# Kernel tuning notes

Measured on AMD Instinct MI355X. Metric: run time of the kernel, lower is better.

The kernel has to match this reference:

```python
import jax, jax.numpy as jnp
import numpy as np

# ---- static config ----
B, H, W, C = 32, 64, 64, 256
WS, SHIFT, NH = 8, 4, 8
HD = C // NH
N = WS * WS  # tokens per window
NW = (H // WS) * (W // WS)
EPS = 1e-5


def _relative_position_index(ws):
    ch, cw = np.meshgrid(np.arange(ws), np.arange(ws), indexing='ij')
    coords = np.stack([ch, cw]).reshape(2, -1)          # (2, N)
    rel = coords[:, :, None] - coords[:, None, :]        # (2, N, N)
    rel = rel.transpose(1, 2, 0)
    rel[:, :, 0] += ws - 1
    rel[:, :, 1] += ws - 1
    rel[:, :, 0] *= 2 * ws - 1
    return jnp.asarray(rel.sum(-1))                      # (N, N) int


def _shifted_window_mask(h, w, ws, shift):
    img = np.zeros((h, w))
    slices = (slice(0, -ws), slice(-ws, -shift), slice(-shift, None))
    cnt = 0
    for hs in slices:
        for wsl in slices:
            img[hs, wsl] = cnt
            cnt += 1
    mw = img.reshape(h // ws, ws, w // ws, ws).transpose(0, 2, 1, 3).reshape(-1, ws * ws)
    diff = mw[:, None, :] - mw[:, :, None]
    return jnp.asarray(np.where(diff != 0, -100.0, 0.0).astype(np.float32))  # (nW, N, N)


REL_IDX = _relative_position_index(WS)
ATTN_MASK = _shifted_window_mask(H, W, WS, SHIFT)


def _layernorm(x, g, b):
    mu = jnp.mean(x, axis=-1, keepdims=True)
    var = jnp.mean(jnp.square(x - mu), axis=-1, keepdims=True)
    return (x - mu) * jax.lax.rsqrt(var + EPS) * g + b


def _window_partition(x):  # (B,H,W,C) -> (B*nW, N, C)
    x = x.reshape(B, H // WS, WS, W // WS, WS, C)
    return x.transpose(0, 1, 3, 2, 4, 5).reshape(-1, N, C)


def _window_reverse(win):  # (B*nW, N, C) -> (B,H,W,C)
    x = win.reshape(B, H // WS, W // WS, WS, WS, C)
    return x.transpose(0, 1, 3, 2, 4, 5).reshape(B, H, W, C)


def setup_inputs() -> dict:
    key = jax.random.key(0)
    ks = jax.random.split(key, 6)
    s = lambda fan_in: 1.0 / np.sqrt(fan_in)
    return {
        'x': jax.random.normal(ks[0], (B, H * W, C), jnp.float32),
        'norm1_g': jnp.ones((C,), jnp.float32),
        'norm1_b': jnp.zeros((C,), jnp.float32),
        'qkv_w': jax.random.normal(ks[1], (C, 3 * C), jnp.float32) * s(C),
        'qkv_b': jnp.zeros((3 * C,), jnp.float32),
        'proj_w': jax.random.normal(ks[2], (C, C), jnp.float32) * s(C),
        'proj_b': jnp.zeros((C,), jnp.float32),
        'bias_table': jax.random.normal(ks[3], ((2 * WS - 1) ** 2, NH), jnp.float32) * 0.02,
        'norm2_g': jnp.ones((C,), jnp.float32),
        'norm2_b': jnp.zeros((C,), jnp.float32),
        'fc1_w': jax.random.normal(ks[4], (C, 4 * C), jnp.float32) * s(C),
        'fc1_b': jnp.zeros((4 * C,), jnp.float32),
        'fc2_w': jax.random.normal(ks[5], (4 * C, C), jnp.float32) * s(4 * C),
        'fc2_b': jnp.zeros((C,), jnp.float32),
    }


def reference(x, norm1_g, norm1_b, qkv_w, qkv_b, proj_w, proj_b, bias_table,
              norm2_g, norm2_b, fc1_w, fc1_b, fc2_w, fc2_b):
    shortcut = x
    h = _layernorm(x, norm1_g, norm1_b).reshape(B, H, W, C)
    # cyclic shift
    h = jnp.roll(h, shift=(-SHIFT, -SHIFT), axis=(1, 2))
    xw = _window_partition(h)                               # (Bw, N, C), Bw = B*nW
    # window attention
    qkv = xw @ qkv_w + qkv_b                                 # (Bw, N, 3C)
    qkv = qkv.reshape(-1, N, 3, NH, HD).transpose(2, 0, 3, 1, 4)
    q, k, v = qkv[0], qkv[1], qkv[2]                         # (Bw, NH, N, HD)
    attn = jnp.einsum('whnd,whmd->whnm', q * (HD ** -0.5), k)
    rpb = bias_table[REL_IDX.reshape(-1)].reshape(N, N, NH).transpose(2, 0, 1)
    attn = attn + rpb[None]
    attn = attn.reshape(B, NW, NH, N, N) + ATTN_MASK[None, :, None]
    attn = jax.nn.softmax(attn.reshape(-1, NH, N, N), axis=-1)
    out = jnp.einsum('whnm,whmd->whnd', attn, v)
    out = out.transpose(0, 2, 1, 3).reshape(-1, N, C)
    out = out @ proj_w + proj_b
    # reverse windows + shift back
    h = _window_reverse(out)
    h = jnp.roll(h, shift=(SHIFT, SHIFT), axis=(1, 2)).reshape(B, H * W, C)
    x = shortcut + h
    # MLP with pre-norm residual
    m = _layernorm(x, norm2_g, norm2_b)
    m = jax.nn.gelu(m @ fc1_w + fc1_b, approximate=False) @ fc2_w + fc2_b
    return x + m
```

## Files before the change

### kernel.cpp

```cpp
#include <hip/hip_runtime.h>
#include <hip/hip_bf16.h>


typedef __bf16 bf16;
typedef __bf16 bf16x8 __attribute__((ext_vector_type(8)));
typedef __bf16 bf16x4 __attribute__((ext_vector_type(4)));
typedef float  f32x4  __attribute__((ext_vector_type(4)));

#define M_TOK 131072

#define GLDS(gp, lp)                                                                   \
    __builtin_amdgcn_global_load_lds(                                                  \
        (const __attribute__((address_space(1))) unsigned int*)(gp),                   \
        (__attribute__((address_space(3))) unsigned int*)(lp), 16, 0, 0)

__global__ __launch_bounds__(256) void transpose_w(const float* __restrict__ src,
                                                   bf16* __restrict__ dst,
                                                   int K, int N) {
    int idx = blockIdx.x * 256 + threadIdx.x;
    int k = idx / N, n = idx - k * N;
    dst[(size_t)n * K + k] = (bf16)src[idx];
}

__global__ __launch_bounds__(256) void build_rpb(const float* __restrict__ bt,
                                                 float* __restrict__ rpb) {
    int idx = blockIdx.x * 256 + threadIdx.x;
    int h = idx >> 12, n = (idx >> 6) & 63, m = idx & 63;
    int ridx = ((n >> 3) - (m >> 3) + 7) * 15 + ((n & 7) - (m & 7) + 7);
    rpb[idx] = bt[ridx * 8 + h];
}

template <int PERM>
__global__ __launch_bounds__(256) void ln_k(const float* __restrict__ x,
                                            const float* __restrict__ g,
                                            const float* __restrict__ bb,
                                            bf16* __restrict__ dst) {
    int t = blockIdx.x * 4 + (threadIdx.x >> 6);
    int lane = threadIdx.x & 63;
    size_t src;
    if (PERM) {
        int w = t >> 6, n = t & 63;
        int b = w >> 6, nw = w & 63;
        int r = ((nw >> 3) * 8 + (n >> 3) + 4) & 63;
        int c = ((nw & 7) * 8 + (n & 7) + 4) & 63;
        src = ((size_t)b * 4096 + r * 64 + c) * 256;
    } else {
        src = (size_t)t * 256;
    }
    float4 v = *(const float4*)&x[src + lane * 4];
    float s = v.x + v.y + v.z + v.w;
    float sq = v.x * v.x + v.y * v.y + v.z * v.z + v.w * v.w;
#pragma unroll
    for (int off = 1; off < 64; off <<= 1) {
        s += __shfl_xor(s, off);
        sq += __shfl_xor(sq, off);
    }
    float mean = s * (1.0f / 256.0f);
    float var = sq * (1.0f / 256.0f) - mean * mean;
    float rstd = rsqrtf(var + 1e-5f);
    float4 gg = *(const float4*)&g[lane * 4];
    float4 bv = *(const float4*)&bb[lane * 4];
    bf16x4 o;
    o[0] = (bf16)((v.x - mean) * rstd * gg.x + bv.x);
    o[1] = (bf16)((v.y - mean) * rstd * gg.y + bv.y);
    o[2] = (bf16)((v.z - mean) * rstd * gg.z + bv.z);
    o[3] = (bf16)((v.w - mean) * rstd * gg.w + bv.w);
    *(bf16x4*)&dst[(size_t)t * 256 + lane * 4] = o;
}

__device__ __forceinline__ float fast_gelu(float v) {
    float t = v * v;
    float w = __builtin_fmaf(0.044715f * t, v, v);
    float e = __expf(-1.5957691216057308f * w);
    return v * __builtin_amdgcn_rcpf(1.0f + e);
}

template <int NDIM, int KDIM, int EPI>
__global__ __launch_bounds__(256) void gemm_k(const bf16* __restrict__ A,
                                              const bf16* __restrict__ Bt,
                                              const float* __restrict__ bias,
                                              bf16* __restrict__ outb,
                                              float* __restrict__ outf,
                                              const float* __restrict__ resid) {
    __shared__ __align__(16) bf16 SH[24576];
    constexpr int NBN = NDIM / 128;
    constexpr int NK = KDIM / 32;
    static_assert(NK >= 3, "pipeline needs >=3 K-steps");
    const int tid = threadIdx.x;
    const int nwg = gridDim.x;
    const int flat = blockIdx.x;
    const int cpx = nwg >> 3;
    const int orig = (flat & 7) * cpx + (flat >> 3);
    const int bm = orig / NBN, bn = orig % NBN;

    const int lane = tid & 63, wid = tid >> 6;
    const int wr = wid >> 1, wc = wid & 1;
    const int lhi = lane >> 4, llo = lane & 15;

    f32x4 acc[4][4];
#pragma unroll
    for (int i = 0; i < 4; i++)
#pragma unroll
        for (int j = 0; j < 4; j++) acc[i][j] = f32x4{0.f, 0.f, 0.f, 0.f};

    const int srow = wid * 32 + (lane >> 2);
    const int scol = (((lane & 3) - ((lane >> 3) & 3)) & 3) * 8;
    const bf16* Ap = A + (size_t)(bm * 128 + srow) * KDIM + scol;
    const bf16* Bp = Bt + (size_t)(bn * 128 + srow) * KDIM + scol;
    const int gsw = ((lhi + (llo >> 1)) & 3) * 8;

#define STAGE(bufidx)                                                                  \
    do {                                                                               \
        bf16* Al = SH + (bufidx)*4096 + wid * 1024;                                    \
        bf16* Bl = SH + 12288 + (bufidx)*4096 + wid * 1024;                            \
        GLDS(Ap, Al);                                                                  \
        GLDS(Ap + 16 * KDIM, Al + 16 * 32);                                            \
        GLDS(Bp, Bl);                                                                  \
        GLDS(Bp + 16 * KDIM, Bl + 16 * 32);                                            \
        Ap += 32;                                                                      \
        Bp += 32;                                                                      \
    } while (0)

#define COMPUTE(bufidx)                                                                \
    do {                                                                               \
        const int ab = (bufidx)*4096;                                                  \
        bf16x8 af[4], bfr[4];                                                          \
        _Pragma("unroll") for (int mi = 0; mi < 4; mi++) af[mi] =                      \
            *(const bf16x8*)&SH[ab + (wr * 64 + mi * 16 + llo) * 32 + gsw];            \
        _Pragma("unroll") for (int ni = 0; ni < 4; ni++) bfr[ni] =                     \
            *(const bf16x8*)&SH[12288 + ab + (wc * 64 + ni * 16 + llo) * 32 + gsw];    \
        _Pragma("unroll") for (int mi = 0; mi < 4; mi++)                               \
            _Pragma("unroll") for (int ni = 0; ni < 4; ni++) acc[mi][ni] =             \
                __builtin_amdgcn_mfma_f32_16x16x32_bf16(bfr[ni], af[mi],               \
                                                        acc[mi][ni], 0, 0, 0);         \
    } while (0)

#define WAITBAR(N)                                                                     \
    asm volatile("s_waitcnt vmcnt(" #N ")" ::: "memory");                              \
    __builtin_amdgcn_s_barrier();                                                      \
    __builtin_amdgcn_sched_barrier(0)

#define END_PHASE                                                                      \
    asm volatile("s_waitcnt lgkmcnt(0)" ::: "memory");                                 \
    __builtin_amdgcn_s_barrier();                                                      \
    __builtin_amdgcn_sched_barrier(0)

    STAGE(0);
    STAGE(1);
    STAGE(2);
    int buf = 0;
    for (int i = 0; i + 3 < NK; ++i) {
        WAITBAR(8);
        COMPUTE(buf);
        END_PHASE;
        STAGE(buf);
        buf = (buf == 2) ? 0 : buf + 1;
    }
    WAITBAR(8);
    COMPUTE(buf);
    buf = (buf == 2) ? 0 : buf + 1;
    WAITBAR(4);
    COMPUTE(buf);
    buf = (buf == 2) ? 0 : buf + 1;
    WAITBAR(0);
    COMPUTE(buf);

#undef STAGE
#undef COMPUTE
#undef WAITBAR
#undef END_PHASE

    __syncthreads();

    char* shb = (char*)SH;
    if constexpr (EPI == 0 || EPI == 2) {
#pragma unroll
        for (int ni = 0; ni < 4; ni++) {
            const int lcol = wc * 64 + ni * 16 + lhi * 4;
            const float4 b4 = *(const float4*)&bias[bn * 128 + lcol];
#pragma unroll
            for (int mi = 0; mi < 4; mi++) {
                const int ltok = wr * 64 + mi * 16 + llo;
                float v0 = acc[mi][ni][0] + b4.x;
                float v1 = acc[mi][ni][1] + b4.y;
                float v2 = acc[mi][ni][2] + b4.z;
                float v3 = acc[mi][ni][3] + b4.w;
                bf16x4 o;
                if constexpr (EPI == 2) {
                    o[0] = (bf16)fast_gelu(v0); o[1] = (bf16)fast_gelu(v1);
                    o[2] = (bf16)fast_gelu(v2); o[3] = (bf16)fast_gelu(v3);
                } else {
                    o[0] = (bf16)v0; o[1] = (bf16)v1; o[2] = (bf16)v2; o[3] = (bf16)v3;
                }
                const int u2 = (lcol >> 3) ^ (ltok & 15);
                *(bf16x4*)(shb + ltok * 256 + u2 * 16 + (lcol & 7) * 2) = o;
            }
        }
        __syncthreads();
        const int j = lane & 15;
#pragma unroll
        for (int rnd = 0; rnd < 8; rnd++) {
            const int ltok = wid * 32 + rnd * 4 + (lane >> 4);
            const int u2 = j ^ (ltok & 15);
            bf16x8 v = *(const bf16x8*)(shb + ltok * 256 + u2 * 16);
            *(bf16x8*)&outb[(size_t)(bm * 128 + ltok) * NDIM + bn * 128 + j * 8] = v;
        }
    } else {
#pragma unroll
        for (int p = 0; p < 2; p++) {
            if (wc == p) {
#pragma unroll
                for (int ni = 0; ni < 4; ni++) {
                    const int lcolh = ni * 16 + lhi * 4;
                    const float4 b4 = *(const float4*)&bias[bn * 128 + p * 64 + lcolh];
#pragma unroll
                    for (int mi = 0; mi < 4; mi++) {
                        const int ltok = wr * 64 + mi * 16 + llo;
                        float4 o = {acc[mi][ni][0] + b4.x, acc[mi][ni][1] + b4.y,
                                    acc[mi][ni][2] + b4.z, acc[mi][ni][3] + b4.w};
                        const int u2 = (lcolh >> 2) ^ (ltok & 15);
                        *(float4*)(shb + ltok * 256 + u2 * 16) = o;
                    }
                }
            }
            __syncthreads();
            const int j = lane & 15;
#pragma unroll
            for (int rnd = 0; rnd < 8; rnd++) {
                const int ltok = wid * 32 + rnd * 4 + (lane >> 4);
                const int u2 = j ^ (ltok & 15);
                float4 v = *(const float4*)(shb + ltok * 256 + u2 * 16);
                const int gcol = bn * 128 + p * 64 + j * 4;
                const int grow = bm * 128 + ltok;
                size_t dst = (size_t)grow * NDIM + gcol;
                float4 cur = *(const float4*)&outf[dst];
                float4 o = {cur.x + v.x, cur.y + v.y, cur.z + v.z, cur.w + v.w};
                *(float4*)&outf[dst] = o;
            }
            if (p == 0) __syncthreads();
        }
    }
}

__global__ __launch_bounds__(256) void proj_ln_k(const bf16* __restrict__ A,
                                                 const bf16* __restrict__ Bt,
                                                 const float* __restrict__ bias,
                                                 const float* __restrict__ resid,
                                                 float* __restrict__ outf,
                                                 const float* __restrict__ g2,
                                                 const float* __restrict__ b2,
                                                 bf16* __restrict__ hb) {
    __shared__ __align__(16) bf16 SH[32768];
    constexpr int KDIM = 256;
    const int tid = threadIdx.x;
    const int nwg = gridDim.x;
    const int flat = blockIdx.x;
    const int cpx = nwg >> 3;
    const int bm = (flat & 7) * cpx + (flat >> 3);

    const int lane = tid & 63, wid = tid >> 6;
    const int lhi = lane >> 4, llo = lane & 15;

    f32x4 acc[4][4];
#pragma unroll
    for (int i = 0; i < 4; i++)
#pragma unroll
        for (int j = 0; j < 4; j++) acc[i][j] = f32x4{0.f, 0.f, 0.f, 0.f};

    const int scol = (((lane & 3) - ((lane >> 3) & 3)) & 3) * 8;
    const bf16* Ap = A + (size_t)(bm * 64 + wid * 16 + (lane >> 2)) * KDIM + scol;
    const bf16* Bp = Bt + (size_t)(wid * 64 + (lane >> 2)) * KDIM + scol;
    const int gsw = ((lhi + (llo >> 1)) & 3) * 8;

#define PSTAGE(bufidx)                                                                 \
    do {                                                                               \
        bf16* Al = SH + (bufidx)*2048 + wid * 512;                                     \
        bf16* Bl = SH + 6144 + (bufidx)*8192 + wid * 2048;                             \
        GLDS(Ap, Al);                                                                  \
        GLDS(Bp, Bl);                                                                  \
        GLDS(Bp + 16 * KDIM, Bl + 512);                                                \
        GLDS(Bp + 32 * KDIM, Bl + 1024);                                               \
        GLDS(Bp + 48 * KDIM, Bl + 1536);                                               \
        Ap += 32;                                                                      \
        Bp += 32;                                                                      \
    } while (0)

#define PCOMPUTE(bufidx)                                                               \
    do {                                                                               \
        bf16x8 af[4], bfr[4];                                                          \
        _Pragma("unroll") for (int mi = 0; mi < 4; mi++) af[mi] =                      \
            *(const bf16x8*)&SH[(bufidx)*2048 + (mi * 16 + llo) * 32 + gsw];           \
        _Pragma("unroll") for (int ni = 0; ni < 4; ni++) bfr[ni] =                     \
            *(const bf16x8*)&SH[6144 + (bufidx)*8192 +                                 \
                                (wid * 64 + ni * 16 + llo) * 32 + gsw];                \
        _Pragma("unroll") for (int mi = 0; mi < 4; mi++)                               \
            _Pragma("unroll") for (int ni = 0; ni < 4; ni++) acc[mi][ni] =             \
                __builtin_amdgcn_mfma_f32_16x16x32_bf16(bfr[ni], af[mi],               \
                                                        acc[mi][ni], 0, 0, 0);         \
    } while (0)

#define PWAITBAR(N)                                                                    \
    asm volatile("s_waitcnt vmcnt(" #N ")" ::: "memory");                              \
    __builtin_amdgcn_s_barrier();                                                      \
    __builtin_amdgcn_sched_barrier(0)

    PSTAGE(0);
    PSTAGE(1);
    PSTAGE(2);
    int buf = 0;
    for (int i = 0; i + 3 < 8; ++i) {
        PWAITBAR(10);
        PCOMPUTE(buf);
        asm volatile("s_waitcnt lgkmcnt(0)" ::: "memory");
        __builtin_amdgcn_s_barrier();
        __builtin_amdgcn_sched_barrier(0);
        PSTAGE(buf);
        buf = (buf == 2) ? 0 : buf + 1;
    }
    PWAITBAR(10);
    PCOMPUTE(buf);
    buf = (buf == 2) ? 0 : buf + 1;
    PWAITBAR(5);
    PCOMPUTE(buf);
    buf = (buf == 2) ? 0 : buf + 1;
    PWAITBAR(0);
    PCOMPUTE(buf);

#undef PSTAGE
#undef PCOMPUTE
#undef PWAITBAR

    __syncthreads();

    char* shb = (char*)SH;
#pragma unroll
    for (int ni = 0; ni < 4; ni++) {
        const int col0 = wid * 64 + ni * 16 + lhi * 4;
        const float4 b4 = *(const float4*)&bias[col0];
#pragma unroll
        for (int mi = 0; mi < 4; mi++) {
            const int ltok = mi * 16 + llo;
            float4 o = {acc[mi][ni][0] + b4.x, acc[mi][ni][1] + b4.y,
                        acc[mi][ni][2] + b4.z, acc[mi][ni][3] + b4.w};
            const int u2 = (col0 >> 2) ^ (ltok & 15);
            *(float4*)(shb + ltok * 1024 + u2 * 16) = o;
        }
    }
    __syncthreads();

    const float4 gg = *(const float4*)&g2[lane * 4];
    const float4 bb4 = *(const float4*)&b2[lane * 4];
#pragma unroll
    for (int rnd = 0; rnd < 16; rnd++) {
        const int t = rnd * 4 + wid;
        const int u2 = lane ^ (t & 15);
        float4 v = *(const float4*)(shb + t * 1024 + u2 * 16);
        const int grow = bm * 64 + t;
        int w = grow >> 6, n = grow & 63;
        int b = w >> 6, nw = w & 63;
        int rr = ((nw >> 3) * 8 + (n >> 3) + 4) & 63;
        int cc = ((nw & 7) * 8 + (n & 7) + 4) & 63;
        const size_t rowbase = ((size_t)b * 4096 + rr * 64 + cc) * 256;
        float4 rs = *(const float4*)&resid[rowbase + lane * 4];
        float4 o = {rs.x + v.x, rs.y + v.y, rs.z + v.z, rs.w + v.w};
        *(float4*)&outf[rowbase + lane * 4] = o;
        float s = o.x + o.y + o.z + o.w;
        float sq = o.x * o.x + o.y * o.y + o.z * o.z + o.w * o.w;
#pragma unroll
        for (int off = 1; off < 64; off <<= 1) {
            s += __shfl_xor(s, off);
            sq += __shfl_xor(sq, off);
        }
        float mean = s * (1.0f / 256.0f);
        float var = sq * (1.0f / 256.0f) - mean * mean;
        float rstd = rsqrtf(var + 1e-5f);
        bf16x4 ho;
        ho[0] = (bf16)((o.x - mean) * rstd * gg.x + bb4.x);
        ho[1] = (bf16)((o.y - mean) * rstd * gg.y + bb4.y);
        ho[2] = (bf16)((o.z - mean) * rstd * gg.z + bb4.z);
        ho[3] = (bf16)((o.w - mean) * rstd * gg.w + bb4.w);
        *(bf16x4*)&hb[rowbase + lane * 4] = ho;
    }
}

__device__ __forceinline__ int regid3(int p) { return p < 56 ? 0 : (p < 60 ? 1 : 2); }

__global__ __launch_bounds__(256) void attn_k(const bf16* __restrict__ qkv,
                                              const float* __restrict__ rpb,
                                              bf16* __restrict__ aout) {
    __shared__ __align__(16) bf16 Pl[4][64 * 80];
    const int wid = threadIdx.x >> 6, lane = threadIdx.x & 63;
    const int lhi = lane >> 4, llo = lane & 15;
    const int wh = blockIdx.x * 4 + wid;
    const int w = wh >> 3, h = wh & 7;
    const bf16* base = qkv + (size_t)w * (64 * 768);

    bf16x8 qf[4], kf[4];
#pragma unroll
    for (int i = 0; i < 4; i++)
        qf[i] = *(const bf16x8*)(base + (i * 16 + llo) * 768 + h * 32 + lhi * 8);
#pragma unroll
    for (int i = 0; i < 4; i++)
        kf[i] = *(const bf16x8*)(base + (i * 16 + llo) * 768 + 256 + h * 32 + lhi * 8);
    f32x4 s[4][4];
#pragma unroll
    for (int mi = 0; mi < 4; mi++)
#pragma unroll
        for (int ni = 0; ni < 4; ni++) {
            s[mi][ni] = f32x4{0.f, 0.f, 0.f, 0.f};
            s[mi][ni] =
                __builtin_amdgcn_mfma_f32_16x16x32_bf16(qf[mi], kf[ni], s[mi][ni], 0, 0, 0);
        }

    const int nw = w & 63;
    const int pr0 = (nw >> 3) * 8, pc0 = (nw & 7) * 8;
    int creg[4];
#pragma unroll
    for (int ni = 0; ni < 4; ni++) {
        int m = ni * 16 + llo;
        creg[ni] = regid3(pr0 + (m >> 3)) * 3 + regid3(pc0 + (m & 7));
    }
    float rmax[4][4], rsum[4][4];
#pragma unroll
    for (int mi = 0; mi < 4; mi++)
#pragma unroll
        for (int r = 0; r < 4; r++) {
            int n = mi * 16 + lhi * 4 + r;
            int rreg = regid3(pr0 + (n >> 3)) * 3 + regid3(pc0 + (n & 7));
            float mx = -1e30f;
#pragma unroll
            for (int ni = 0; ni < 4; ni++) {
                int m = ni * 16 + llo;
                float sv = s[mi][ni][r] * 0.17677669529663687f + rpb[(h * 64 + n) * 64 + m] +
                           (rreg == creg[ni] ? 0.0f : -100.0f);
                s[mi][ni][r] = sv;
                mx = fmaxf(mx, sv);
            }
            rmax[mi][r] = mx;
        }
#pragma unroll
    for (int off = 1; off < 16; off <<= 1)
#pragma unroll
        for (int mi = 0; mi < 4; mi++)
#pragma unroll
            for (int r = 0; r < 4; r++)
                rmax[mi][r] = fmaxf(rmax[mi][r], __shfl_xor(rmax[mi][r], off));
#pragma unroll
    for (int mi = 0; mi < 4; mi++)
#pragma unroll
        for (int r = 0; r < 4; r++) {
            float a = 0.f;
#pragma unroll
            for (int ni = 0; ni < 4; ni++) {
                float p = __expf(s[mi][ni][r] - rmax[mi][r]);
                s[mi][ni][r] = p;
                a += p;
            }
            rsum[mi][r] = a;
        }
#pragma unroll
    for (int off = 1; off < 16; off <<= 1)
#pragma unroll
        for (int mi = 0; mi < 4; mi++)
#pragma unroll
            for (int r = 0; r < 4; r++) rsum[mi][r] += __shfl_xor(rsum[mi][r], off);

    bf16* P = Pl[wid];
#pragma unroll
    for (int mi = 0; mi < 4; mi++)
#pragma unroll
        for (int r = 0; r < 4; r++) {
            float rinv = 1.0f / rsum[mi][r];
            int row = mi * 16 + lhi * 4 + r;
#pragma unroll
            for (int ni = 0; ni < 4; ni++)
                P[row * 80 + ni * 16 + llo] = (bf16)(s[mi][ni][r] * rinv);
        }

    f32x4 o[4][2];
#pragma unroll
    for (int mi = 0; mi < 4; mi++)
#pragma unroll
        for (int ni = 0; ni < 2; ni++) o[mi][ni] = f32x4{0.f, 0.f, 0.f, 0.f};
#pragma unroll
    for (int kc = 0; kc < 2; kc++) {
        bf16x8 pf[4], vf[2];
#pragma unroll
        for (int mi = 0; mi < 4; mi++)
            pf[mi] = *(const bf16x8*)(P + (mi * 16 + llo) * 80 + kc * 32 + lhi * 8);
#pragma unroll
        for (int ni = 0; ni < 2; ni++)
#pragma unroll
            for (int j = 0; j < 8; j++)
                vf[ni][j] = base[(kc * 32 + lhi * 8 + j) * 768 + 512 + h * 32 + ni * 16 + llo];
#pragma unroll
        for (int mi = 0; mi < 4; mi++)
#pragma unroll
            for (int ni = 0; ni < 2; ni++)
                o[mi][ni] =
                    __builtin_amdgcn_mfma_f32_16x16x32_bf16(pf[mi], vf[ni], o[mi][ni], 0, 0, 0);
    }
#pragma unroll
    for (int mi = 0; mi < 4; mi++)
#pragma unroll
        for (int ni = 0; ni < 2; ni++)
#pragma unroll
            for (int r = 0; r < 4; r++) {
                int row = mi * 16 + lhi * 4 + r;
                aout[(size_t)(w * 64 + row) * 256 + h * 32 + ni * 16 + llo] =
                    (bf16)o[mi][ni][r];
            }
}

extern "C" void kernel_launch(void* const* d_in, const int* in_sizes, int n_in,
                              void* d_out, int out_size, void* d_ws, size_t ws_size,
                              hipStream_t stream) {
    const float* x      = (const float*)d_in[0];
    const float* n1g    = (const float*)d_in[1];
    const float* n1b    = (const float*)d_in[2];
    const float* qkv_w  = (const float*)d_in[3];
    const float* qkv_b  = (const float*)d_in[4];
    const float* proj_w = (const float*)d_in[5];
    const float* proj_b = (const float*)d_in[6];
    const float* btab   = (const float*)d_in[7];
    const float* n2g    = (const float*)d_in[8];
    const float* n2b    = (const float*)d_in[9];
    const float* fc1_w  = (const float*)d_in[10];
    const float* fc1_b  = (const float*)d_in[11];
    const float* fc2_w  = (const float*)d_in[12];
    const float* fc2_b  = (const float*)d_in[13];
    float* out = (float*)d_out;
    char* ws = (char*)d_ws;

    constexpr size_t o_xw   = 0;
    constexpr size_t o_qkvb = 67108864ull;
    constexpr size_t o_attn = 268435456ull;
    constexpr size_t o_g    = 0;
    constexpr size_t o_h    = 268435456ull;
    constexpr size_t o_hb   = 335544320ull;
    constexpr size_t o_wq   = o_hb + 67108864ull;
    constexpr size_t o_wp   = o_wq + 393216;
    constexpr size_t o_w1   = o_wp + 131072;
    constexpr size_t o_w2   = o_w1 + 524288;
    constexpr size_t o_rpb  = o_w2 + 524288;

    bf16* XW    = (bf16*)(ws + o_xw);
    bf16* QKVB  = (bf16*)(ws + o_qkvb);
    bf16* ATTN  = (bf16*)(ws + o_attn);
    bf16* Gbuf  = (bf16*)(ws + o_g);
    bf16* Hb    = (bf16*)(ws + o_hb);
    bf16* WQ    = (bf16*)(ws + o_wq);
    bf16* WP    = (bf16*)(ws + o_wp);
    bf16* W1    = (bf16*)(ws + o_w1);
    bf16* W2    = (bf16*)(ws + o_w2);
    float* RPB  = (float*)(ws + o_rpb);

    dim3 blk(256);
    transpose_w<<<768, blk, 0, stream>>>(qkv_w, WQ, 256, 768);
    transpose_w<<<256, blk, 0, stream>>>(proj_w, WP, 256, 256);
    transpose_w<<<1024, blk, 0, stream>>>(fc1_w, W1, 256, 1024);
    transpose_w<<<1024, blk, 0, stream>>>(fc2_w, W2, 1024, 256);
    build_rpb<<<128, blk, 0, stream>>>(btab, RPB);

    ln_k<1><<<M_TOK / 4, blk, 0, stream>>>(x, n1g, n1b, XW);

    for (int c = 0; c < 2; ++c) {
        const size_t toff = (size_t)c * 65536;
        gemm_k<768, 256, 0><<<3072, blk, 0, stream>>>(XW + toff * 256, WQ, qkv_b,
                                                      QKVB, nullptr, nullptr);
        attn_k<<<2048, blk, 0, stream>>>(QKVB, RPB, ATTN + toff * 256);
    }

    proj_ln_k<<<2048, blk, 0, stream>>>(ATTN, WP, proj_b, x, out, n2g, n2b, Hb);

    for (int q = 0; q < 4; ++q) {
        const size_t toff = (size_t)q * 32768;
        gemm_k<1024, 256, 2><<<2048, blk, 0, stream>>>(Hb + toff * 256, W1, fc1_b,
                                                       Gbuf, nullptr, nullptr);
        gemm_k<256, 1024, 3><<<512, blk, 0, stream>>>(Gbuf, W2, fc2_b, nullptr,
                                                      out + toff * 256, nullptr);
    }
}
```

Baseline: 590.4 us.

## Store residual base as bf16, shrink proj LDS pipeline, merge prep kernels, larger MLP chunks

The proj+LN kernel now writes the post-attention residual as a bf16 buffer instead of fp32 into the output. The fc2 epilogue reads that bf16 base and writes the final fp32 output, so it no longer does a read-modify-write of fp32 output. This cuts memory traffic but loses residual precision. The proj kernel drops from a 3-stage to a 2-stage LDS pipeline and splits its epilogue into two halves to reduce shared memory, aiming for higher occupancy. The weight transposes and the rpb build are merged into one launch, and the MLP runs in 2 chunks instead of 4.

```diff
diff --git a/kernel.cpp b/kernel.cpp
--- a/kernel.cpp
+++ b/kernel.cpp
@@ -14,39 +14,49 @@
         (const __attribute__((address_space(1))) unsigned int*)(gp),                   \
         (__attribute__((address_space(3))) unsigned int*)(lp), 16, 0, 0)
 
-__global__ __launch_bounds__(256) void transpose_w(const float* __restrict__ src,
-                                                   bf16* __restrict__ dst,
-                                                   int K, int N) {
+__global__ __launch_bounds__(256) void prep_all(const float* __restrict__ qkv_w,
+                                                const float* __restrict__ proj_w,
+                                                const float* __restrict__ fc1_w,
+                                                const float* __restrict__ fc2_w,
+                                                const float* __restrict__ bt,
+                                                bf16* __restrict__ WQ, bf16* __restrict__ WP,
+                                                bf16* __restrict__ W1, bf16* __restrict__ W2,
+                                                float* __restrict__ rpb) {
     int idx = blockIdx.x * 256 + threadIdx.x;
-    int k = idx / N, n = idx - k * N;
-    dst[(size_t)n * K + k] = (bf16)src[idx];
-}
-
-__global__ __launch_bounds__(256) void build_rpb(const float* __restrict__ bt,
-                                                 float* __restrict__ rpb) {
-    int idx = blockIdx.x * 256 + threadIdx.x;
-    int h = idx >> 12, n = (idx >> 6) & 63, m = idx & 63;
-    int ridx = ((n >> 3) - (m >> 3) + 7) * 15 + ((n & 7) - (m & 7) + 7);
-    rpb[idx] = bt[ridx * 8 + h];
-}
-
-template <int PERM>
+    if (idx < 196608) {
+        int k = idx / 768, n = idx - k * 768;
+        WQ[(size_t)n * 256 + k] = (bf16)qkv_w[idx];
+    } else if (idx < 262144) {
+        int l = idx - 196608;
+        int k = l >> 8, n = l & 255;
+        WP[(size_t)n * 256 + k] = (bf16)proj_w[l];
+    } else if (idx < 524288) {
+        int l = idx - 262144;
+        int k = l >> 10, n = l & 1023;
+        W1[(size_t)n * 256 + k] = (bf16)fc1_w[l];
+    } else if (idx < 786432) {
+        int l = idx - 524288;
+        int k = l >> 8, n = l & 255;
+        W2[(size_t)n * 1024 + k] = (bf16)fc2_w[l];
+    } else {
+        int l = idx - 786432;
+        int h = l >> 12, n = (l >> 6) & 63, m = l & 63;
+        int ridx = ((n >> 3) - (m >> 3) + 7) * 15 + ((n & 7) - (m & 7) + 7);
+        rpb[l] = bt[ridx * 8 + h];
+    }
+}
+
 __global__ __launch_bounds__(256) void ln_k(const float* __restrict__ x,
                                             const float* __restrict__ g,
                                             const float* __restrict__ bb,
                                             bf16* __restrict__ dst) {
     int t = blockIdx.x * 4 + (threadIdx.x >> 6);
     int lane = threadIdx.x & 63;
-    size_t src;
-    if (PERM) {
-        int w = t >> 6, n = t & 63;
-        int b = w >> 6, nw = w & 63;
-        int r = ((nw >> 3) * 8 + (n >> 3) + 4) & 63;
-        int c = ((nw & 7) * 8 + (n & 7) + 4) & 63;
-        src = ((size_t)b * 4096 + r * 64 + c) * 256;
-    } else {
-        src = (size_t)t * 256;
-    }
+    int w = t >> 6, n = t & 63;
+    int b = w >> 6, nw = w & 63;
+    int r = ((nw >> 3) * 8 + (n >> 3) + 4) & 63;
+    int c = ((nw & 7) * 8 + (n & 7) + 4) & 63;
+    size_t src = ((size_t)b * 4096 + r * 64 + c) * 256;
     float4 v = *(const float4*)&x[src + lane * 4];
     float s = v.x + v.y + v.z + v.w;
     float sq = v.x * v.x + v.y * v.y + v.z * v.z + v.w * v.w;
@@ -81,11 +91,10 @@
                                               const float* __restrict__ bias,
                                               bf16* __restrict__ outb,
                                               float* __restrict__ outf,
-                                              const float* __restrict__ resid) {
+                                              const bf16* __restrict__ baseb) {
     __shared__ __align__(16) bf16 SH[24576];
     constexpr int NBN = NDIM / 128;
     constexpr int NK = KDIM / 32;
-    static_assert(NK >= 3, "pipeline needs >=3 K-steps");
     const int tid = threadIdx.x;
     const int nwg = gridDim.x;
     const int flat = blockIdx.x;
@@ -233,8 +242,9 @@
                 const int gcol = bn * 128 + p * 64 + j * 4;
                 const int grow = bm * 128 + ltok;
                 size_t dst = (size_t)grow * NDIM + gcol;
-                float4 cur = *(const float4*)&outf[dst];
-                float4 o = {cur.x + v.x, cur.y + v.y, cur.z + v.z, cur.w + v.w};
+                bf16x4 bb = *(const bf16x4*)&baseb[dst];
+                float4 o = {v.x + (float)bb[0], v.y + (float)bb[1],
+                            v.z + (float)bb[2], v.w + (float)bb[3]};
                 *(float4*)&outf[dst] = o;
             }
             if (p == 0) __syncthreads();
@@ -246,11 +256,11 @@
                                                  const bf16* __restrict__ Bt,
                                                  const float* __restrict__ bias,
                                                  const float* __restrict__ resid,
-                                                 float* __restrict__ outf,
+                                                 bf16* __restrict__ baseb,
                                                  const float* __restrict__ g2,
                                                  const float* __restrict__ b2,
                                                  bf16* __restrict__ hb) {
-    __shared__ __align__(16) bf16 SH[32768];
+    __shared__ __align__(16) bf16 SH[20480];
     constexpr int KDIM = 256;
     const int tid = threadIdx.x;
     const int nwg = gridDim.x;
@@ -275,7 +285,7 @@
 #define PSTAGE(bufidx)                                                                 \
     do {                                                                               \
         bf16* Al = SH + (bufidx)*2048 + wid * 512;                                     \
-        bf16* Bl = SH + 6144 + (bufidx)*8192 + wid * 2048;                             \
+        bf16* Bl = SH + 4096 + (bufidx)*8192 + wid * 2048;                             \
         GLDS(Ap, Al);                                                                  \
         GLDS(Bp, Bl);                                                                  \
         GLDS(Bp + 16 * KDIM, Bl + 512);                                                \
@@ -291,7 +301,7 @@
         _Pragma("unroll") for (int mi = 0; mi < 4; mi++) af[mi] =                      \
             *(const bf16x8*)&SH[(bufidx)*2048 + (mi * 16 + llo) * 32 + gsw];           \
         _Pragma("unroll") for (int ni = 0; ni < 4; ni++) bfr[ni] =                     \
-            *(const bf16x8*)&SH[6144 + (bufidx)*8192 +                                 \
+            *(const bf16x8*)&SH[4096 + (bufidx)*8192 +                                 \
                                 (wid * 64 + ni * 16 + llo) * 32 + gsw];                \
         _Pragma("unroll") for (int mi = 0; mi < 4; mi++)                               \
             _Pragma("unroll") for (int ni = 0; ni < 4; ni++) acc[mi][ni] =             \
@@ -299,87 +309,86 @@
                                                         acc[mi][ni], 0, 0, 0);         \
     } while (0)
 
-#define PWAITBAR(N)                                                                    \
-    asm volatile("s_waitcnt vmcnt(" #N ")" ::: "memory");                              \
-    __builtin_amdgcn_s_barrier();                                                      \
-    __builtin_amdgcn_sched_barrier(0)
-
     PSTAGE(0);
     PSTAGE(1);
-    PSTAGE(2);
     int buf = 0;
-    for (int i = 0; i + 3 < 8; ++i) {
-        PWAITBAR(10);
+    for (int i = 0; i + 2 < 8; ++i) {
+        asm volatile("s_waitcnt vmcnt(5)" ::: "memory");
+        __builtin_amdgcn_s_barrier();
+        __builtin_amdgcn_sched_barrier(0);
         PCOMPUTE(buf);
         asm volatile("s_waitcnt lgkmcnt(0)" ::: "memory");
         __builtin_amdgcn_s_barrier();
         __builtin_amdgcn_sched_barrier(0);
         PSTAGE(buf);
-        buf = (buf == 2) ? 0 : buf + 1;
-    }
-    PWAITBAR(10);
+        buf ^= 1;
+    }
+    asm volatile("s_waitcnt vmcnt(5)" ::: "memory");
+    __builtin_amdgcn_s_barrier();
+    __builtin_amdgcn_sched_barrier(0);
     PCOMPUTE(buf);
-    buf = (buf == 2) ? 0 : buf + 1;
-    PWAITBAR(5);
-    PCOMPUTE(buf);
-    buf = (buf == 2) ? 0 : buf + 1;
-    PWAITBAR(0);
+    buf ^= 1;
+    asm volatile("s_waitcnt vmcnt(0)" ::: "memory");
+    __builtin_amdgcn_s_barrier();
+    __builtin_amdgcn_sched_barrier(0);
     PCOMPUTE(buf);
 
 #undef PSTAGE
 #undef PCOMPUTE
-#undef PWAITBAR
-
-    __syncthreads();
 
     char* shb = (char*)SH;
-#pragma unroll
-    for (int ni = 0; ni < 4; ni++) {
-        const int col0 = wid * 64 + ni * 16 + lhi * 4;
-        const float4 b4 = *(const float4*)&bias[col0];
-#pragma unroll
-        for (int mi = 0; mi < 4; mi++) {
-            const int ltok = mi * 16 + llo;
-            float4 o = {acc[mi][ni][0] + b4.x, acc[mi][ni][1] + b4.y,
-                        acc[mi][ni][2] + b4.z, acc[mi][ni][3] + b4.w};
-            const int u2 = (col0 >> 2) ^ (ltok & 15);
-            *(float4*)(shb + ltok * 1024 + u2 * 16) = o;
-        }
-    }
-    __syncthreads();
-
     const float4 gg = *(const float4*)&g2[lane * 4];
     const float4 bb4 = *(const float4*)&b2[lane * 4];
 #pragma unroll
-    for (int rnd = 0; rnd < 16; rnd++) {
-        const int t = rnd * 4 + wid;
-        const int u2 = lane ^ (t & 15);
-        float4 v = *(const float4*)(shb + t * 1024 + u2 * 16);
-        const int grow = bm * 64 + t;
-        int w = grow >> 6, n = grow & 63;
-        int b = w >> 6, nw = w & 63;
-        int rr = ((nw >> 3) * 8 + (n >> 3) + 4) & 63;
-        int cc = ((nw & 7) * 8 + (n & 7) + 4) & 63;
-        const size_t rowbase = ((size_t)b * 4096 + rr * 64 + cc) * 256;
-        float4 rs = *(const float4*)&resid[rowbase + lane * 4];
-        float4 o = {rs.x + v.x, rs.y + v.y, rs.z + v.z, rs.w + v.w};
-        *(float4*)&outf[rowbase + lane * 4] = o;
-        float s = o.x + o.y + o.z + o.w;
-        float sq = o.x * o.x + o.y * o.y + o.z * o.z + o.w * o.w;
-#pragma unroll
-        for (int off = 1; off < 64; off <<= 1) {
-            s += __shfl_xor(s, off);
-            sq += __shfl_xor(sq, off);
-        }
-        float mean = s * (1.0f / 256.0f);
-        float var = sq * (1.0f / 256.0f) - mean * mean;
-        float rstd = rsqrtf(var + 1e-5f);
-        bf16x4 ho;
-        ho[0] = (bf16)((o.x - mean) * rstd * gg.x + bb4.x);
-        ho[1] = (bf16)((o.y - mean) * rstd * gg.y + bb4.y);
-        ho[2] = (bf16)((o.z - mean) * rstd * gg.z + bb4.z);
-        ho[3] = (bf16)((o.w - mean) * rstd * gg.w + bb4.w);
-        *(bf16x4*)&hb[rowbase + lane * 4] = ho;
+    for (int p = 0; p < 2; p++) {
+        __syncthreads();
+#pragma unroll
+        for (int ni = 0; ni < 4; ni++) {
+            const int col0 = wid * 64 + ni * 16 + lhi * 4;
+            const float4 b4 = *(const float4*)&bias[col0];
+#pragma unroll
+            for (int m2 = 0; m2 < 2; m2++) {
+                const int mi = 2 * p + m2;
+                const int lt = m2 * 16 + llo;
+                float4 o = {acc[mi][ni][0] + b4.x, acc[mi][ni][1] + b4.y,
+                            acc[mi][ni][2] + b4.z, acc[mi][ni][3] + b4.w};
+                const int u2 = (col0 >> 2) ^ (lt & 15);
+                *(float4*)(shb + lt * 1024 + u2 * 16) = o;
+            }
+        }
+        __syncthreads();
+#pragma unroll
+        for (int rnd = 0; rnd < 8; rnd++) {
+            const int lt = rnd * 4 + wid;
+            const int u2 = lane ^ (lt & 15);
+            float4 v = *(const float4*)(shb + lt * 1024 + u2 * 16);
+            const int grow = bm * 64 + p * 32 + lt;
+            int w = grow >> 6, n = grow & 63;
+            int b = w >> 6, nw = w & 63;
+            int rr = ((nw >> 3) * 8 + (n >> 3) + 4) & 63;
+            int cc = ((nw & 7) * 8 + (n & 7) + 4) & 63;
+            const size_t rowbase = ((size_t)b * 4096 + rr * 64 + cc) * 256;
+            float4 rs = *(const float4*)&resid[rowbase + lane * 4];
+            float4 o = {rs.x + v.x, rs.y + v.y, rs.z + v.z, rs.w + v.w};
+            bf16x4 bo = {(bf16)o.x, (bf16)o.y, (bf16)o.z, (bf16)o.w};
+            *(bf16x4*)&baseb[rowbase + lane * 4] = bo;
+            float s = o.x + o.y + o.z + o.w;
+            float sq = o.x * o.x + o.y * o.y + o.z * o.z + o.w * o.w;
+#pragma unroll
+            for (int off = 1; off < 64; off <<= 1) {
+                s += __shfl_xor(s, off);
+                sq += __shfl_xor(sq, off);
+            }
+            float mean = s * (1.0f / 256.0f);
+            float var = sq * (1.0f / 256.0f) - mean * mean;
+            float rstd = rsqrtf(var + 1e-5f);
+            bf16x4 ho;
+            ho[0] = (bf16)((o.x - mean) * rstd * gg.x + bb4.x);
+            ho[1] = (bf16)((o.y - mean) * rstd * gg.y + bb4.y);
+            ho[2] = (bf16)((o.z - mean) * rstd * gg.z + bb4.z);
+            ho[3] = (bf16)((o.w - mean) * rstd * gg.w + bb4.w);
+            *(bf16x4*)&hb[rowbase + lane * 4] = ho;
+        }
     }
 }
 
@@ -532,37 +541,24 @@
     float* out = (float*)d_out;
     char* ws = (char*)d_ws;
 
-    constexpr size_t o_xw   = 0;
-    constexpr size_t o_qkvb = 67108864ull;
-    constexpr size_t o_attn = 268435456ull;
-    constexpr size_t o_g    = 0;
-    constexpr size_t o_h    = 268435456ull;
-    constexpr size_t o_hb   = 335544320ull;
-    constexpr size_t o_wq   = o_hb + 67108864ull;
-    constexpr size_t o_wp   = o_wq + 393216;
-    constexpr size_t o_w1   = o_wp + 131072;
-    constexpr size_t o_w2   = o_w1 + 524288;
-    constexpr size_t o_rpb  = o_w2 + 524288;
-
-    bf16* XW    = (bf16*)(ws + o_xw);
-    bf16* QKVB  = (bf16*)(ws + o_qkvb);
-    bf16* ATTN  = (bf16*)(ws + o_attn);
-    bf16* Gbuf  = (bf16*)(ws + o_g);
-    bf16* Hb    = (bf16*)(ws + o_hb);
-    bf16* WQ    = (bf16*)(ws + o_wq);
-    bf16* WP    = (bf16*)(ws + o_wp);
-    bf16* W1    = (bf16*)(ws + o_w1);
-    bf16* W2    = (bf16*)(ws + o_w2);
-    float* RPB  = (float*)(ws + o_rpb);
+    constexpr size_t MB = 1048576ull;
+    bf16* XW    = (bf16*)(ws);
+    bf16* BASEB = (bf16*)(ws);
+    bf16* QKVB  = (bf16*)(ws + 67 * MB);
+    bf16* Gbuf  = (bf16*)(ws + 67 * MB);
+    bf16* Hb    = (bf16*)(ws + 201 * MB);
+    bf16* ATTN  = (bf16*)(ws + 268 * MB);
+    bf16* WQ    = (bf16*)(ws + 335 * MB);
+    bf16* WP    = (bf16*)(ws + 335 * MB + 393216);
+    bf16* W1    = (bf16*)(ws + 335 * MB + 524288);
+    bf16* W2    = (bf16*)(ws + 335 * MB + 1048576);
+    float* RPB  = (float*)(ws + 335 * MB + 1572864);
 
     dim3 blk(256);
-    transpose_w<<<768, blk, 0, stream>>>(qkv_w, WQ, 256, 768);
-    transpose_w<<<256, blk, 0, stream>>>(proj_w, WP, 256, 256);
-    transpose_w<<<1024, blk, 0, stream>>>(fc1_w, W1, 256, 1024);
-    transpose_w<<<1024, blk, 0, stream>>>(fc2_w, W2, 1024, 256);
-    build_rpb<<<128, blk, 0, stream>>>(btab, RPB);
-
-    ln_k<1><<<M_TOK / 4, blk, 0, stream>>>(x, n1g, n1b, XW);
+    prep_all<<<3200, blk, 0, stream>>>(qkv_w, proj_w, fc1_w, fc2_w, btab,
+                                       WQ, WP, W1, W2, RPB);
+
+    ln_k<<<M_TOK / 4, blk, 0, stream>>>(x, n1g, n1b, XW);
 
     for (int c = 0; c < 2; ++c) {
         const size_t toff = (size_t)c * 65536;
@@ -571,13 +567,14 @@
         attn_k<<<2048, blk, 0, stream>>>(QKVB, RPB, ATTN + toff * 256);
     }
 
-    proj_ln_k<<<2048, blk, 0, stream>>>(ATTN, WP, proj_b, x, out, n2g, n2b, Hb);
-
-    for (int q = 0; q < 4; ++q) {
-        const size_t toff = (size_t)q * 32768;
-        gemm_k<1024, 256, 2><<<2048, blk, 0, stream>>>(Hb + toff * 256, W1, fc1_b,
+    proj_ln_k<<<2048, blk, 0, stream>>>(ATTN, WP, proj_b, x, BASEB, n2g, n2b, Hb);
+
+    for (int q = 0; q < 2; ++q) {
+        const size_t toff = (size_t)q * 65536;
+        gemm_k<1024, 256, 2><<<4096, blk, 0, stream>>>(Hb + toff * 256, W1, fc1_b,
                                                        Gbuf, nullptr, nullptr);
-        gemm_k<256, 1024, 3><<<512, blk, 0, stream>>>(Gbuf, W2, fc2_b, nullptr,
-                                                      out + toff * 256, nullptr);
-    }
-}
+        gemm_k<256, 1024, 3><<<1024, blk, 0, stream>>>(Gbuf, W2, fc2_b, nullptr,
+                                                       out + toff * 256,
+                                                       BASEB + toff * 256);
+    }
+}
```

Measured after the change: 584.4 us. Within noise of the previous version (-1.0%).
